# Performance work log

Measured on AMD Instinct MI355X. Metric: run time of the kernel, lower is better.

## Reference

```python
import jax, jax.numpy as jnp
import numpy as np

WSZ = 2
ZNEAR, ZFAR = 0.1, 100.0


def _grid_sample_bilinear(img, gx, gy):
    # img [H,W]; gx,gy [n] normalized coords in [-1,1]
    # matches torch F.grid_sample(mode='bilinear', padding_mode='zeros', align_corners=True)
    H, W = img.shape
    ix = (gx + 1.0) * 0.5 * (W - 1)
    iy = (gy + 1.0) * 0.5 * (H - 1)
    x0 = jnp.floor(ix)
    y0 = jnp.floor(iy)
    wx = ix - x0
    wy = iy - y0
    x0i = x0.astype(jnp.int32)
    y0i = y0.astype(jnp.int32)

    def tap(xi, yi):
        v = (xi >= 0) & (xi < W) & (yi >= 0) & (yi < H)
        return img[jnp.clip(yi, 0, H - 1), jnp.clip(xi, 0, W - 1)] * v

    return (tap(x0i, y0i) * (1 - wx) * (1 - wy)
            + tap(x0i + 1, y0i) * wx * (1 - wy)
            + tap(x0i, y0i + 1) * (1 - wx) * wy
            + tap(x0i + 1, y0i + 1) * wx * wy)


def _forward(alpha, beta, pp, conf, pose_w2c, K):
    b, _, n = pp.shape
    h, w = alpha.shape[-2:]
    H2, W2 = h * WSZ, w * WSZ

    # project points: pc = pose_w2c @ pp[:, :4]
    pc = jnp.einsum('bij,bjn->bin', pose_w2c, pp[:, :4])  # [b,4,n]
    z = jnp.abs(pc[:, 2])
    xc = pc[:, 0] * K[:, 0, 0][:, None] / z + K[:, 0, 2][:, None]
    yc = pc[:, 1] * K[:, 1, 1][:, None] / z + K[:, 1, 2][:, None]

    gx = xc / float(w - 1) * 2.0 - 1.0
    gy = -(yc / float(h - 1) * 2.0 - 1.0)
    conf_sampled = jax.vmap(_grid_sample_bilinear)(beta[:, 0], gx, gy)[:, None]  # [b,1,n]

    xs = jnp.round(xc * WSZ).astype(jnp.int32)
    ys = jnp.round(yc * WSZ).astype(jnp.int32)
    oob = ((xs < 0) | (xs >= W2) | (ys < 0) | (ys >= H2)
           | (z < ZNEAR) | (z > ZFAR) | (conf <= 0))
    valid = ~oob

    alpha_up = jnp.repeat(jnp.repeat(alpha[:, 0], WSZ, axis=-1), WSZ, axis=-2)[:, ::-1, :]

    idx_pts = jnp.arange(n, dtype=jnp.int32)
    row_base = jnp.arange(h)[:, None] * WSZ
    col_base = jnp.arange(w)[None, :] * WSZ

    def one(conf_b, xs_b, ys_b, valid_b, alpha_b):
        # scatter conf / point-index into hi-res z-buffer (invalid -> dropped)
        flat = jnp.where(valid_b, ys_b * W2 + xs_b, H2 * W2)
        cmap = jnp.zeros(H2 * W2, conf_b.dtype).at[flat].set(conf_b, mode='drop').reshape(H2, W2)
        idxh = jnp.full(H2 * W2, -1, jnp.int32).at[flat].set(idx_pts, mode='drop').reshape(H2, W2)
        keep = (alpha_b > 0) & (cmap > 0)
        cm = cmap * keep
        # 2x2 max-pool with indices
        win = cm.reshape(h, WSZ, w, WSZ).transpose(0, 2, 1, 3).reshape(h, w, WSZ * WSZ)
        a = jnp.argmax(win, axis=-1)  # [h,w] in 0..3
        rows = row_base + a // WSZ
        cols = col_base + a % WSZ
        idxh = jnp.where(keep, idxh, -1)
        idx_sel = idxh[rows, cols]
        match = keep.astype(cm.dtype).reshape(h, WSZ, w, WSZ).max(axis=(1, 3))
        return match[::-1], idx_sel[::-1]

    match, midx = jax.vmap(one)(conf, xs, ys, valid, alpha_up)
    return match[:, None], midx[:, None], conf_sampled


def setup_inputs() -> dict:
    key = jax.random.key(0)
    ks = jax.random.split(key, 8)
    b, h, w = 8, 480, 640
    n = h * w
    fx = fy = 500.0
    cx, cy = (w - 1) / 2.0, (h - 1) / 2.0
    # back-project uniformly sampled pixels/depths -> geometrically valid cloud
    u = jax.random.uniform(ks[0], (b, n), minval=0.0, maxval=w - 1.0)
    v = jax.random.uniform(ks[1], (b, n), minval=0.0, maxval=h - 1.0)
    zz = jax.random.uniform(ks[2], (b, n), minval=0.5, maxval=10.0)
    X = (u - cx) * zz / fx
    Y = (v - cy) * zz / fy
    rgb = jax.random.uniform(ks[3], (b, 3, n))
    pp = jnp.concatenate([jnp.stack([X, Y, zz, jnp.ones_like(zz)], axis=1), rgb], axis=1).astype(jnp.float32)
    pose_w2c = jnp.tile(jnp.eye(4, dtype=jnp.float32), (b, 1, 1))
    K = jnp.tile(jnp.array([[fx, 0.0, cx], [0.0, fy, cy], [0.0, 0.0, 1.0]], jnp.float32), (b, 1, 1))
    alpha = (jax.random.uniform(ks[4], (b, 1, h, w)) > 0.05).astype(jnp.float32)
    beta = jax.random.uniform(ks[5], (b, 1, h, w))
    conf = jax.random.uniform(ks[6], (b, n), minval=-0.1, maxval=1.0)
    return {"alpha": alpha, "beta": beta, "pp": pp, "conf": conf,
            "pose_w2c": pose_w2c, "K": K, "h": h, "w": w}


def reference(alpha, beta, pp, conf, pose_w2c, K, h, w):
    # h, w are ignored by the original module (re-read from alpha)
    return _forward(alpha, beta, pp, conf, pose_w2c, K)
```

## Files before the change

### kernel.cpp

```cpp
#include <hip/hip_runtime.h>

#define WSZ 2
#define ZNEAR 0.1f
#define ZFAR 100.0f
#define NT 256
#define CHUNK 2048
#define KPT (CHUNK / NT)
#define MAXBINS 8192
#define THIST 256
#define CSTRIDE 16

__device__ __forceinline__ void derive_geom(int h, int w, int n,
                                            int& H2, int& W2, int& rpt,
                                            int& cpt, int& tpb, bool& ok) {
    H2 = h * WSZ; W2 = w * WSZ;
    rpt = (W2 > 0) ? ((MAXBINS / W2) & ~1) : 2;
    if (rpt < 2) rpt = 2;
    if (rpt > H2) rpt = H2;
    cpt = rpt * W2;
    tpb = (H2 + rpt - 1) / rpt;
    ok = (cpt <= MAXBINS) && (tpb <= THIST) && (n <= (1 << 19)) && (W2 <= 8192);
}

__global__ void zero_kernel(int* __restrict__ p, int total) {
    int t = blockIdx.x * blockDim.x + threadIdx.x;
    if (t < total) p[t] = 0;
}

__global__ void __launch_bounds__(NT)
project_bin_kernel(const float* __restrict__ pp,
                   const float* __restrict__ conf,
                   const float* __restrict__ pose,
                   const float* __restrict__ Kmat,
                   const float* __restrict__ beta,
                   const int* __restrict__ d_h,
                   const int* __restrict__ d_w,
                   int* __restrict__ counters,
                   unsigned int* __restrict__ records,
                   float* __restrict__ out_conf,
                   int n, int b, int cap) {
    __shared__ unsigned int staging[CHUNK];
    __shared__ int hist[THIST];
    __shared__ int scan[THIST];
    __shared__ int segstart[THIST];
    __shared__ int cursor[THIST];
    __shared__ int gbase[THIST];

    const int h = *d_h, w = *d_w;
    int H2, W2, rpt, cpt, tpb; bool geom_ok;
    derive_geom(h, w, n, H2, W2, rpt, cpt, tpb, geom_ok);

    const int b_idx = blockIdx.x % b;
    const int off   = (blockIdx.x / b) * CHUNK;
    const int tid   = threadIdx.x;

    hist[tid] = 0;
    __syncthreads();

    const float* P  = pose + b_idx * 16;
    const float* Kb = Kmat + b_idx * 9;
    const float fxk = Kb[0], cxk = Kb[2], fyk = Kb[4], cyk = Kb[5];
    const float p00 = P[0], p01 = P[1], p02 = P[2],  p03 = P[3];
    const float p10 = P[4], p11 = P[5], p12 = P[6],  p13 = P[7];
    const float p20 = P[8], p21 = P[9], p22 = P[10], p23 = P[11];
    const float* B = beta + (size_t)b_idx * h * w;

    unsigned int words[KPT];

    #pragma unroll
    for (int k = 0; k < KPT; ++k) {
        words[k] = 0xFFFFFFFFu;
        int i = off + k * NT + tid;
        if (i >= n) continue;

        const float* ppb = pp + (size_t)b_idx * 7 * n + i;
        float px = ppb[0];
        float py = ppb[(size_t)n];
        float pz = ppb[(size_t)2 * n];
        float pw = ppb[(size_t)3 * n];

        float pc0 = p00 * px + p01 * py + p02 * pz + p03 * pw;
        float pc1 = p10 * px + p11 * py + p12 * pz + p13 * pw;
        float pc2 = p20 * px + p21 * py + p22 * pz + p23 * pw;

        float z = fabsf(pc2);
        float xc = pc0 * fxk / z + cxk;
        float yc = pc1 * fyk / z + cyk;

        float gx = xc / (float)(w - 1) * 2.0f - 1.0f;
        float gy = -(yc / (float)(h - 1) * 2.0f - 1.0f);
        float ix = (gx + 1.0f) * 0.5f * (float)(w - 1);
        float iy = (gy + 1.0f) * 0.5f * (float)(h - 1);
        float cs = 0.0f;
        if (ix > -1.0f && ix < (float)w && iy > -1.0f && iy < (float)h) {
            float x0f = floorf(ix), y0f = floorf(iy);
            float wx = ix - x0f, wy = iy - y0f;
            int x0 = (int)x0f, y0 = (int)y0f;
            float t00 = 0.0f, t10 = 0.0f, t01 = 0.0f, t11 = 0.0f;
            if (y0 >= 0 && y0 < h) {
                const float* R = B + (size_t)y0 * w;
                if (x0 >= 0 && x0 < w)         t00 = R[x0];
                if (x0 + 1 >= 0 && x0 + 1 < w) t10 = R[x0 + 1];
            }
            if (y0 + 1 >= 0 && y0 + 1 < h) {
                const float* R = B + (size_t)(y0 + 1) * w;
                if (x0 >= 0 && x0 < w)         t01 = R[x0];
                if (x0 + 1 >= 0 && x0 + 1 < w) t11 = R[x0 + 1];
            }
            cs = t00 * (1.0f - wx) * (1.0f - wy)
               + t10 * wx * (1.0f - wy)
               + t01 * (1.0f - wx) * wy
               + t11 * wx * wy;
        }
        out_conf[(size_t)b_idx * n + i] = cs;

        float cf = conf[(size_t)b_idx * n + i];
        float rx = rintf(xc * (float)WSZ);
        float ry = rintf(yc * (float)WSZ);
        bool valid = (rx >= 0.0f) && (rx < (float)W2) &&
                     (ry >= 0.0f) && (ry < (float)H2) &&
                     (z >= ZNEAR) && (z <= ZFAR) && (cf > 0.0f);
        if (valid && geom_ok) {
            int xs = (int)rx, ys = (int)ry;
            int ty = (int)((unsigned)ys / (unsigned)rpt);
            int cib = (ys - ty * rpt) * W2 + xs;
            words[k] = ((unsigned)ty << 13) | (unsigned)cib;
            atomicAdd(&hist[ty], 1);
        }
    }
    __syncthreads();

    int own = hist[tid];
    scan[tid] = own;
    __syncthreads();
    #pragma unroll
    for (int s = 1; s < THIST; s <<= 1) {
        int v = (tid >= s) ? scan[tid - s] : 0;
        __syncthreads();
        scan[tid] += v;
        __syncthreads();
    }
    int sstart = scan[tid] - own;
    segstart[tid] = sstart;
    cursor[tid] = sstart;
    gbase[tid] = (tid < tpb && own > 0)
               ? atomicAdd(&counters[(b_idx * tpb + tid) * CSTRIDE], own) : 0;
    __syncthreads();

    #pragma unroll
    for (int k = 0; k < KPT; ++k) {
        unsigned int word = words[k];
        if (word == 0xFFFFFFFFu) continue;
        int ty = (int)(word >> 13);
        unsigned int cib = word & 8191u;
        int i = off + k * NT + tid;
        int slot = atomicAdd(&cursor[ty], 1);
        staging[slot] = (cib << 19) | (unsigned)i;
    }
    __syncthreads();

    const int wave = tid >> 6, lane = tid & 63;
    for (int t = wave; t < tpb; t += NT / 64) {
        int ss = segstart[t];
        int cnt = cursor[t] - ss;
        if (cnt <= 0) continue;
        int gb = gbase[t];
        int allowed = cap - gb; if (allowed < 0) allowed = 0;
        if (cnt > allowed) cnt = allowed;
        unsigned int* dst = records + (size_t)(b_idx * tpb + t) * cap + gb;
        for (int j = lane; j < cnt; j += 64) dst[j] = staging[ss + j];
    }
}

__global__ void __launch_bounds__(NT)
pool_bins_kernel(const float* __restrict__ alpha,
                 const float* __restrict__ conf,
                 const int* __restrict__ counters,
                 const unsigned int* __restrict__ records,
                 const int* __restrict__ d_h,
                 const int* __restrict__ d_w,
                 float* __restrict__ out_match,
                 float* __restrict__ out_midx,
                 int b, int n, int hw, int cap) {
    __shared__ int cells[MAXBINS];
    const int h = *d_h, w = *d_w;
    int H2, W2, rpt, cpt, tpb; bool geom_ok;
    derive_geom(h, w, n, H2, W2, rpt, cpt, tpb, geom_ok);
    if (!geom_ok) return;

    const int b_idx = blockIdx.x % b;
    const int ty    = blockIdx.x / b;
    if (ty >= tpb) return;
    const int bin = b_idx * tpb + ty;

    for (int i = threadIdx.x; i < MAXBINS; i += NT) cells[i] = -1;
    __syncthreads();

    int cnt = counters[bin * CSTRIDE];
    if (cnt > cap) cnt = cap;
    const unsigned int* rec = records + (size_t)bin * cap;
    for (int r = threadIdx.x; r < cnt; r += NT) {
        unsigned int rr = rec[r];
        atomicMax(&cells[rr >> 19], (int)(rr & 0x7FFFFu));
    }
    __syncthreads();

    const int row0 = ty * rpt;
    int rmax = H2 - row0; if (rmax > rpt) rmax = rpt;
    const float* A = alpha + (size_t)b_idx * hw;
    const float* C = conf + (size_t)b_idx * n;

    for (int q = 0; q < rmax / 2; ++q) {
        int hr = (row0 >> 1) + q;
        int r_out = h - 1 - hr;
        for (int c = threadIdx.x; c < w; c += NT) {
            float av = A[r_out * w + c];
            float best = 0.0f;
            int besti = -1;
            if (av > 0.0f) {
                #pragma unroll
                for (int a = 0; a < 4; ++a) {
                    int dy = a >> 1, dx = a & 1;
                    int widx = cells[(2 * q + dy) * W2 + 2 * c + dx];
                    if (widx >= 0) {
                        float cv = C[widx];
                        if (cv > best) { best = cv; besti = widx; }
                    }
                }
            }
            int o = b_idx * hw + r_out * w + c;
            out_match[o] = (best > 0.0f) ? 1.0f : 0.0f;
            out_midx[o]  = (float)besti;
        }
    }
}

extern "C" void kernel_launch(void* const* d_in, const int* in_sizes, int n_in,
                              void* d_out, int out_size, void* d_ws, size_t ws_size,
                              hipStream_t stream) {
    const float* alpha = (const float*)d_in[0];
    const float* beta  = (const float*)d_in[1];
    const float* pp    = (const float*)d_in[2];
    const float* conf  = (const float*)d_in[3];
    const float* pose  = (const float*)d_in[4];
    const float* Kmat  = (const float*)d_in[5];
    const int*   d_h   = (const int*)d_in[6];
    const int*   d_w   = (const int*)d_in[7];

    const int b  = in_sizes[4] / 16;
    const int n  = in_sizes[3] / b;
    const int hw = in_sizes[0] / b;

    float* out_match = (float*)d_out;
    float* out_midx  = out_match + (size_t)b * hw;
    float* out_conf  = out_midx + (size_t)b * hw;

    const int nb_ub = b * (4 * hw / 4096 + 2);

    long avail_ints = (long)(ws_size / 4) - (long)nb_ub * CSTRIDE;
    long cap_l = avail_ints / (nb_ub > 0 ? nb_ub : 1);
    int cap = (int)cap_l;
    if (cap > 4096) cap = 4096;
    if (cap < 64) cap = 64;

    int* counters = (int*)d_ws;
    unsigned int* records = (unsigned int*)(counters + (size_t)nb_ub * CSTRIDE);

    const int cnt_total = nb_ub * CSTRIDE;
    zero_kernel<<<(cnt_total + NT - 1) / NT, NT, 0, stream>>>(counters, cnt_total);

    const int bpb = (n + CHUNK - 1) / CHUNK;
    project_bin_kernel<<<b * bpb, NT, 0, stream>>>(
        pp, conf, pose, Kmat, beta, d_h, d_w,
        counters, records, out_conf, n, b, cap);

    pool_bins_kernel<<<nb_ub, NT, 0, stream>>>(
        alpha, conf, counters, records, d_h, d_w,
        out_match, out_midx, b, n, hw, cap);
}
```

Measured before the change: 98.25 us.

## Batch point loads in groups, vectorize bilinear taps, use wave-shuffle scan

The projection loop now processes points in groups of four. All global loads for a group are issued before the dependent beta gathers, and the gathers before the interpolation and binning math, which exposes more memory-level parallelism per thread. When the column index is even and in range, the two horizontal bilinear taps are fetched with one float2 load. The 256-entry histogram scan, which used shared memory with a barrier at every step, becomes a wave-level shuffle scan plus a small cross-wave sum. The trade-off is higher register pressure from holding four points' state at once.

```diff
diff --git a/kernel.cpp b/kernel.cpp
--- a/kernel.cpp
+++ b/kernel.cpp
@@ -6,6 +6,7 @@
 #define NT 256
 #define CHUNK 2048
 #define KPT (CHUNK / NT)
+#define GRP 4
 #define MAXBINS 8192
 #define THIST 256
 #define CSTRIDE 16
@@ -41,10 +42,10 @@
                    int n, int b, int cap) {
     __shared__ unsigned int staging[CHUNK];
     __shared__ int hist[THIST];
-    __shared__ int scan[THIST];
     __shared__ int segstart[THIST];
     __shared__ int cursor[THIST];
     __shared__ int gbase[THIST];
+    __shared__ int wsum[NT / 64];
 
     const int h = *d_h, w = *d_w;
     int H2, W2, rpt, cpt, tpb; bool geom_ok;
@@ -66,81 +67,123 @@
     const float* B = beta + (size_t)b_idx * h * w;
 
     unsigned int words[KPT];
-
-    #pragma unroll
-    for (int k = 0; k < KPT; ++k) {
-        words[k] = 0xFFFFFFFFu;
-        int i = off + k * NT + tid;
-        if (i >= n) continue;
-
-        const float* ppb = pp + (size_t)b_idx * 7 * n + i;
-        float px = ppb[0];
-        float py = ppb[(size_t)n];
-        float pz = ppb[(size_t)2 * n];
-        float pw = ppb[(size_t)3 * n];
-
-        float pc0 = p00 * px + p01 * py + p02 * pz + p03 * pw;
-        float pc1 = p10 * px + p11 * py + p12 * pz + p13 * pw;
-        float pc2 = p20 * px + p21 * py + p22 * pz + p23 * pw;
-
-        float z = fabsf(pc2);
-        float xc = pc0 * fxk / z + cxk;
-        float yc = pc1 * fyk / z + cyk;
-
-        float gx = xc / (float)(w - 1) * 2.0f - 1.0f;
-        float gy = -(yc / (float)(h - 1) * 2.0f - 1.0f);
-        float ix = (gx + 1.0f) * 0.5f * (float)(w - 1);
-        float iy = (gy + 1.0f) * 0.5f * (float)(h - 1);
-        float cs = 0.0f;
-        if (ix > -1.0f && ix < (float)w && iy > -1.0f && iy < (float)h) {
-            float x0f = floorf(ix), y0f = floorf(iy);
-            float wx = ix - x0f, wy = iy - y0f;
-            int x0 = (int)x0f, y0 = (int)y0f;
-            float t00 = 0.0f, t10 = 0.0f, t01 = 0.0f, t11 = 0.0f;
+    #pragma unroll
+    for (int k = 0; k < KPT; ++k) words[k] = 0xFFFFFFFFu;
+
+    #pragma unroll
+    for (int g = 0; g < KPT; g += GRP) {
+        float xc_[GRP], yc_[GRP], z_[GRP], cf_[GRP], ix_[GRP], iy_[GRP];
+        bool act_[GRP], sok_[GRP];
+
+        #pragma unroll
+        for (int q = 0; q < GRP; ++q) {
+            int k = g + q;
+            int i = off + k * NT + tid;
+            bool act = (i < n);
+            act_[q] = act;
+            float px = 0.f, py = 0.f, pz = 0.f, pw = 0.f, cf = 0.f;
+            if (act) {
+                const float* ppb = pp + (size_t)b_idx * 7 * n + i;
+                px = ppb[0];
+                py = ppb[(size_t)n];
+                pz = ppb[(size_t)2 * n];
+                pw = ppb[(size_t)3 * n];
+                cf = conf[(size_t)b_idx * n + i];
+            }
+            float pc0 = p00 * px + p01 * py + p02 * pz + p03 * pw;
+            float pc1 = p10 * px + p11 * py + p12 * pz + p13 * pw;
+            float pc2 = p20 * px + p21 * py + p22 * pz + p23 * pw;
+            float z = fabsf(pc2);
+            float xc = pc0 * fxk / z + cxk;
+            float yc = pc1 * fyk / z + cyk;
+            float gx = xc / (float)(w - 1) * 2.0f - 1.0f;
+            float gy = -(yc / (float)(h - 1) * 2.0f - 1.0f);
+            float ix = (gx + 1.0f) * 0.5f * (float)(w - 1);
+            float iy = (gy + 1.0f) * 0.5f * (float)(h - 1);
+            xc_[q] = xc; yc_[q] = yc; z_[q] = z; cf_[q] = cf;
+            ix_[q] = ix; iy_[q] = iy;
+            sok_[q] = act && (ix > -1.0f) && (ix < (float)w)
+                          && (iy > -1.0f) && (iy < (float)h);
+        }
+
+        float t00[GRP], t10[GRP], t01[GRP], t11[GRP];
+        #pragma unroll
+        for (int q = 0; q < GRP; ++q) {
+            t00[q] = t10[q] = t01[q] = t11[q] = 0.0f;
+            if (!sok_[q]) continue;
+            int x0 = (int)floorf(ix_[q]);
+            int y0 = (int)floorf(iy_[q]);
+            bool pair = (x0 >= 0) && (x0 + 1 < w) && ((x0 & 1) == 0);
             if (y0 >= 0 && y0 < h) {
                 const float* R = B + (size_t)y0 * w;
-                if (x0 >= 0 && x0 < w)         t00 = R[x0];
-                if (x0 + 1 >= 0 && x0 + 1 < w) t10 = R[x0 + 1];
+                if (pair) {
+                    float2 p2 = *reinterpret_cast<const float2*>(R + x0);
+                    t00[q] = p2.x; t10[q] = p2.y;
+                } else {
+                    if (x0 >= 0 && x0 < w)         t00[q] = R[x0];
+                    if (x0 + 1 >= 0 && x0 + 1 < w) t10[q] = R[x0 + 1];
+                }
             }
             if (y0 + 1 >= 0 && y0 + 1 < h) {
                 const float* R = B + (size_t)(y0 + 1) * w;
-                if (x0 >= 0 && x0 < w)         t01 = R[x0];
-                if (x0 + 1 >= 0 && x0 + 1 < w) t11 = R[x0 + 1];
-            }
-            cs = t00 * (1.0f - wx) * (1.0f - wy)
-               + t10 * wx * (1.0f - wy)
-               + t01 * (1.0f - wx) * wy
-               + t11 * wx * wy;
+                if (pair) {
+                    float2 p2 = *reinterpret_cast<const float2*>(R + x0);
+                    t01[q] = p2.x; t11[q] = p2.y;
+                } else {
+                    if (x0 >= 0 && x0 < w)         t01[q] = R[x0];
+                    if (x0 + 1 >= 0 && x0 + 1 < w) t11[q] = R[x0 + 1];
+                }
+            }
         }
-        out_conf[(size_t)b_idx * n + i] = cs;
-
-        float cf = conf[(size_t)b_idx * n + i];
-        float rx = rintf(xc * (float)WSZ);
-        float ry = rintf(yc * (float)WSZ);
-        bool valid = (rx >= 0.0f) && (rx < (float)W2) &&
-                     (ry >= 0.0f) && (ry < (float)H2) &&
-                     (z >= ZNEAR) && (z <= ZFAR) && (cf > 0.0f);
-        if (valid && geom_ok) {
-            int xs = (int)rx, ys = (int)ry;
-            int ty = (int)((unsigned)ys / (unsigned)rpt);
-            int cib = (ys - ty * rpt) * W2 + xs;
-            words[k] = ((unsigned)ty << 13) | (unsigned)cib;
-            atomicAdd(&hist[ty], 1);
+
+        #pragma unroll
+        for (int q = 0; q < GRP; ++q) {
+            int k = g + q;
+            int i = off + k * NT + tid;
+            if (!act_[q]) continue;
+            float cs = 0.0f;
+            if (sok_[q]) {
+                float x0f = floorf(ix_[q]), y0f = floorf(iy_[q]);
+                float wx = ix_[q] - x0f, wy = iy_[q] - y0f;
+                cs = t00[q] * (1.0f - wx) * (1.0f - wy)
+                   + t10[q] * wx * (1.0f - wy)
+                   + t01[q] * (1.0f - wx) * wy
+                   + t11[q] * wx * wy;
+            }
+            out_conf[(size_t)b_idx * n + i] = cs;
+
+            float rx = rintf(xc_[q] * (float)WSZ);
+            float ry = rintf(yc_[q] * (float)WSZ);
+            bool valid = (rx >= 0.0f) && (rx < (float)W2) &&
+                         (ry >= 0.0f) && (ry < (float)H2) &&
+                         (z_[q] >= ZNEAR) && (z_[q] <= ZFAR) && (cf_[q] > 0.0f);
+            if (valid && geom_ok) {
+                int xs = (int)rx, ys = (int)ry;
+                int ty = (int)((unsigned)ys / (unsigned)rpt);
+                int cib = (ys - ty * rpt) * W2 + xs;
+                words[k] = ((unsigned)ty << 13) | (unsigned)cib;
+                atomicAdd(&hist[ty], 1);
+            }
         }
     }
     __syncthreads();
 
+    const int lane = tid & 63, wv = tid >> 6;
     int own = hist[tid];
-    scan[tid] = own;
-    __syncthreads();
-    #pragma unroll
-    for (int s = 1; s < THIST; s <<= 1) {
-        int v = (tid >= s) ? scan[tid - s] : 0;
-        __syncthreads();
-        scan[tid] += v;
-        __syncthreads();
-    }
-    int sstart = scan[tid] - own;
+    int v = own;
+    #pragma unroll
+    for (int s = 1; s < 64; s <<= 1) {
+        int u = __shfl_up(v, s, 64);
+        if (lane >= s) v += u;
+    }
+    if (lane == 63) wsum[wv] = v;
+    __syncthreads();
+    int basew = 0;
+    #pragma unroll
+    for (int t = 0; t < NT / 64; ++t)
+        if (t < wv) basew += wsum[t];
+    int incl = basew + v;
+    int sstart = incl - own;
     segstart[tid] = sstart;
     cursor[tid] = sstart;
     gbase[tid] = (tid < tpb && own > 0)
@@ -159,8 +202,7 @@
     }
     __syncthreads();
 
-    const int wave = tid >> 6, lane = tid & 63;
-    for (int t = wave; t < tpb; t += NT / 64) {
+    for (int t = wv; t < tpb; t += NT / 64) {
         int ss = segstart[t];
         int cnt = cursor[t] - ss;
         if (cnt <= 0) continue;
```

New measurement: 93.59 us. 1.05x faster.
